# Kernel tuning notes

Measured on AMD Instinct MI355X. Metric: run time of the kernel, lower is better.

Reference implementation:

```python
import jax, jax.numpy as jnp
import numpy as np
from jax import lax

B, CI, CO, H, W = 8, 64, 64, 256, 256
M1 = M2 = 16
RANK, NEXP, SCALING = 4, 15, 0.1
G = 4  # expert_region_size = sqrt(num_experts + 1)
WF = W // 2 + 1

# expert i occupies grid cell (row, col) = ((i+1)//G, (i+1)%G); cell (0,0) is the base weights1 corner
_IDX = np.arange(1, NEXP + 1)
RR = jnp.asarray(_IDX // G)
CC = jnp.asarray(_IDX % G)


def setup_inputs() -> dict:
    key = jax.random.key(0)
    ks = jax.random.split(key, 20)
    rn = lambda k, shape, s: jax.random.normal(k, shape, jnp.float32) * s
    scale = 1.0 / (CI * CO)
    return {
        "x": rn(ks[0], (B, CI, H, W), 1.0),
        "w1_re": jax.random.uniform(ks[1], (CI, CO, M1, M2), jnp.float32) * scale,
        "w1_im": jax.random.uniform(ks[2], (CI, CO, M1, M2), jnp.float32) * scale,
        "w2_re": jax.random.uniform(ks[3], (CI, CO, M1, M2), jnp.float32) * scale,
        "w2_im": jax.random.uniform(ks[4], (CI, CO, M1, M2), jnp.float32) * scale,
        "la1_re": rn(ks[5], (NEXP, RANK, CI), 0.02),
        "la1_im": rn(ks[6], (NEXP, RANK, CI), 0.02),
        "lb1_re": rn(ks[7], (NEXP, CO, RANK, M1, M2), 0.02),
        "lb1_im": rn(ks[8], (NEXP, CO, RANK, M1, M2), 0.02),
        "la2_re": rn(ks[9], (NEXP, RANK, CI), 0.02),
        "la2_im": rn(ks[10], (NEXP, RANK, CI), 0.02),
        "lb2_re": rn(ks[11], (NEXP, CO, RANK, M1, M2), 0.02),
        "lb2_im": rn(ks[12], (NEXP, CO, RANK, M1, M2), 0.02),
        "gate1": rn(ks[13], (NEXP,), 0.1),
        "gate2": rn(ks[14], (NEXP,), 0.1),
    }


def reference(x, w1_re, w1_im, w2_re, w2_im,
              la1_re, la1_im, lb1_re, lb1_im,
              la2_re, la2_im, lb2_re, lb2_im,
              gate1, gate2):
    x_ft = jnp.fft.rfft2(x)  # [B, CI, H, WF] complex64

    # scalar gates (gate_on_data=False): sigmoid(gate / temperature), temperature=1
    g1 = jax.nn.sigmoid(gate1)  # [E]
    g2 = jax.nn.sigmoid(gate2)
    sploss = jnp.mean(g1) + jnp.mean(g2)

    w1 = lax.complex(w1_re, w1_im)
    w2 = lax.complex(w2_re, w2_im)
    la1 = lax.complex(la1_re, la1_im)
    lb1 = lax.complex(lb1_re, lb1_im)
    la2 = lax.complex(la2_re, la2_im)
    lb2 = lax.complex(lb2_re, lb2_im)

    # per-expert LoRA weights: sum_r lora_b[o,r,x,y] * lora_a[r,i] -> [E, I, O, M1, M2]
    lw1 = jnp.einsum("eri,eorxy->eioxy", la1, lb1) * SCALING
    lw2 = jnp.einsum("eri,eorxy->eioxy", la2, lb2) * SCALING

    # base corner products
    top_base = jnp.einsum("bixy,ioxy->boxy", x_ft[:, :, :M1, :M2], w1)
    bot_base = jnp.einsum("bixy,ioxy->boxy", x_ft[:, :, H - M1:, :M2], w2)

    # gather all expert input tiles at once via a GxG grid view of the low-freq corners
    top = x_ft[:, :, :G * M1, :G * M2].reshape(B, CI, G, M1, G, M2)
    topt = jnp.transpose(top, (2, 4, 0, 1, 3, 5))        # [G, G, B, CI, M1, M2]
    xe1 = topt[RR, CC]                                    # [E, B, CI, M1, M2]
    bot = x_ft[:, :, H - G * M1:, :G * M2].reshape(B, CI, G, M1, G, M2)
    bott = jnp.transpose(bot, (2, 4, 0, 1, 3, 5))
    xe2 = bott[G - 1 - RR, CC]  # rows H-row_end:H-row_start == bottom-grid block 3-row_idx

    oe1 = jnp.einsum("ebixy,eioxy->eboxy", xe1, lw1) * g1[:, None, None, None, None]
    oe2 = jnp.einsum("ebixy,eioxy->eboxy", xe2, lw2) * g2[:, None, None, None, None]

    # scatter all disjoint tiles back into out_ft
    out_top = jnp.zeros((G, G, B, CO, M1, M2), jnp.complex64)
    out_top = out_top.at[0, 0].set(top_base).at[RR, CC].set(oe1)
    out_bot = jnp.zeros((G, G, B, CO, M1, M2), jnp.complex64)
    out_bot = out_bot.at[G - 1, 0].set(bot_base).at[G - 1 - RR, CC].set(oe2)

    out_ft = jnp.zeros((B, CO, H, WF), jnp.complex64)
    top_full = jnp.transpose(out_top, (2, 3, 0, 4, 1, 5)).reshape(B, CO, G * M1, G * M2)
    bot_full = jnp.transpose(out_bot, (2, 3, 0, 4, 1, 5)).reshape(B, CO, G * M1, G * M2)
    out_ft = out_ft.at[:, :, :G * M1, :G * M2].set(top_full)
    out_ft = out_ft.at[:, :, H - G * M1:, :G * M2].set(bot_full)

    y = jnp.fft.irfft2(out_ft, s=(H, W))
    return (y, sploss)
```

## Files before the change

### kernel.cpp

```cpp
#include <hip/hip_runtime.h>
#include <math.h>

#define B_   8
#define CI_  64
#define CO_  64
#define H_   256
#define W_   256
#define NE_  15
#define RK_  4

typedef __attribute__((ext_vector_type(8))) short short8;
typedef __attribute__((ext_vector_type(4))) float f32x4;

__device__ __forceinline__ unsigned bf16u(float f) {
  return (__float_as_uint(f) + 0x8000u) >> 16;
}
__device__ __forceinline__ unsigned pk2(float lo, float hi) {
  return ((__float_as_uint(lo) + 0x8000u) >> 16) |
         ((__float_as_uint(hi) + 0x8000u) & 0xFFFF0000u);
}
__device__ __forceinline__ float ubf(unsigned short u) {
  return __uint_as_float(((unsigned)u) << 16);
}

__global__ __launch_bounds__(256) void kTab(unsigned short* __restrict__ TAt,
                                            unsigned short* __restrict__ TB,
                                            unsigned short* __restrict__ TD,
                                            unsigned short* __restrict__ TEt) {
  int idx = blockIdx.x * 256 + threadIdx.x;
  const float C = 6.28318530717958647692f / 256.f;
  if (idx < 32768) {
    int n = idx >> 8, q = idx & 255;
    int w = n >> 1, pl = n & 1;
    int mm = (q * w) & 255;
    float s, c; sincosf(C * (float)mm, &s, &c);
    TAt[idx] = (unsigned short)bf16u(pl ? -s : c);
    return;
  }
  idx -= 32768;
  if (idx < 131072) {
    int mrow = idx >> 9, k = idx & 511;
    int p = k >> 1, tt = k & 1;
    int hr = mrow & 127, imr = mrow >> 7;
    int h = (hr < 64) ? hr : hr + 128;
    int mm = (p * h) & 255;
    float s, c; sincosf(C * (float)mm, &s, &c);
    float v = (imr == 0) ? (tt == 0 ? c : s) : (tt == 0 ? -s : c);
    TB[idx] = (unsigned short)bf16u(v);
    return;
  }
  idx -= 131072;
  if (idx < 131072) {
    int mrow = idx >> 8, k = idx & 255;
    int hr = k >> 1, tt = k & 1;
    int p = mrow & 255, imr = mrow >> 8;
    int h = (hr < 64) ? hr : hr + 128;
    int mm = (p * h) & 255;
    float s, c; sincosf(C * (float)mm, &s, &c);
    float v = (imr == 0) ? (tt == 0 ? c : -s) : (tt == 0 ? s : c);
    TD[idx] = (unsigned short)bf16u(v);
    return;
  }
  idx -= 131072;
  if (idx < 32768) {
    int q = idx >> 7, k = idx & 127;
    int w = k >> 1, pl = k & 1;
    int mm = (q * w) & 255;
    float s, c; sincosf(C * (float)mm, &s, &c);
    float v = (pl == 0) ? ((w == 0 ? 1.f : 2.f * c) / 65536.f)
                        : ((w == 0 ? 0.f : -2.f * s) / 65536.f);
    TEt[idx] = (unsigned short)bf16u(v);
  }
}

__global__ __launch_bounds__(512, 4) void kAB(const float* __restrict__ x,
                                              const unsigned short* __restrict__ TAt,
                                              const unsigned short* __restrict__ TB,
                                              unsigned short* __restrict__ Xf) {
  __shared__ unsigned short As[256 * 32];
  __shared__ unsigned short Bs1[128 * 32];
  __shared__ unsigned short XcL[64 * 264];
  int t = threadIdx.x, lane = t & 63, wid = t >> 6;
  int bi = blockIdx.x;
  const float* xb = x + (size_t)bi * 65536;
  int lrow = lane & 15, lk = (lane >> 4) * 8;
  f32x4 acc2[2][4];
#pragma unroll
  for (int a = 0; a < 2; ++a)
#pragma unroll
    for (int b = 0; b < 4; ++b) acc2[a][b] = (f32x4){0.f, 0.f, 0.f, 0.f};

  for (int half = 0; half < 2; ++half) {
    f32x4 acc1[2][4];
#pragma unroll
    for (int a = 0; a < 2; ++a)
#pragma unroll
      for (int b = 0; b < 4; ++b) acc1[a][b] = (f32x4){0.f, 0.f, 0.f, 0.f};
    int mb1 = (wid >> 1) * 32, nb1 = (wid & 1) * 64;
    for (int kk = 0; kk < 8; ++kk) {
      int k0 = kk * 32;
      __syncthreads();
      {
        int r = t >> 2, hf = t & 3;
        const float* xp = xb + (size_t)(half * 128 + r) * 256 + k0 + hf * 8;
        float4 v0 = *(const float4*)(xp);
        float4 v1 = *(const float4*)(xp + 4);
        uint4 o;
        o.x = pk2(v0.x, v0.y); o.y = pk2(v0.z, v0.w);
        o.z = pk2(v1.x, v1.y); o.w = pk2(v1.z, v1.w);
        *(uint4*)&As[r * 32 + hf * 8] = o;
      }
      {
        int n = t >> 2, seg = t & 3;
        *(uint4*)&Bs1[n * 32 + seg * 8] = *(const uint4*)&TAt[n * 256 + k0 + seg * 8];
      }
      __syncthreads();
      short8 af[2], bf[4];
#pragma unroll
      for (int a = 0; a < 2; ++a)
        af[a] = *(const short8*)&As[(mb1 + a * 16 + lrow) * 32 + lk];
#pragma unroll
      for (int b = 0; b < 4; ++b)
        bf[b] = *(const short8*)&Bs1[(nb1 + b * 16 + lrow) * 32 + lk];
#pragma unroll
      for (int a = 0; a < 2; ++a)
#pragma unroll
        for (int b = 0; b < 4; ++b)
          acc1[a][b] = __builtin_amdgcn_mfma_f32_16x16x32_bf16(af[a], bf[b], acc1[a][b], 0, 0, 0);
    }
    __syncthreads();
#pragma unroll
    for (int a = 0; a < 2; ++a)
#pragma unroll
      for (int b = 0; b < 4; ++b)
#pragma unroll
        for (int r = 0; r < 4; ++r) {
          int m = mb1 + a * 16 + (lane >> 4) * 4 + r;
          int n = nb1 + b * 16 + lrow;
          XcL[(n >> 1) * 264 + 2 * m + (n & 1)] = (unsigned short)bf16u(acc1[a][b][r]);
        }
    __syncthreads();
    int mb2 = wid * 32;
    for (int kk = 0; kk < 8; ++kk) {
      int k0 = kk * 32;
      __syncthreads();
#pragma unroll
      for (int j = 0; j < 2; ++j) {
        int c = j * 512 + t;
        int m = c >> 2, seg = c & 3;
        *(uint4*)&As[m * 32 + seg * 8] =
            *(const uint4*)&TB[m * 512 + half * 256 + k0 + seg * 8];
      }
      __syncthreads();
      short8 af2[2], bf2[4];
#pragma unroll
      for (int a = 0; a < 2; ++a)
        af2[a] = *(const short8*)&As[(mb2 + a * 16 + lrow) * 32 + lk];
#pragma unroll
      for (int b = 0; b < 4; ++b)
        bf2[b] = *(const short8*)&XcL[(b * 16 + lrow) * 264 + k0 + lk];
#pragma unroll
      for (int a = 0; a < 2; ++a)
#pragma unroll
        for (int b = 0; b < 4; ++b)
          acc2[a][b] = __builtin_amdgcn_mfma_f32_16x16x32_bf16(af2[a], bf2[b], acc2[a][b], 0, 0, 0);
    }
  }
  unsigned short* dst = Xf + (size_t)bi * 16384;
#pragma unroll
  for (int a = 0; a < 2; ++a)
#pragma unroll
    for (int b = 0; b < 4; ++b)
#pragma unroll
      for (int r = 0; r < 4; ++r) {
        int m = wid * 32 + a * 16 + (lane >> 4) * 4 + r;
        int n = b * 16 + lrow;
        dst[m * 64 + n] = (unsigned short)bf16u(acc2[a][b][r]);
      }
}

__global__ __launch_bounds__(256) void kT(const unsigned short* __restrict__ Xf,
                                          float2* __restrict__ T,
                                          const float* __restrict__ la1re,
                                          const float* __restrict__ la1im,
                                          const float* __restrict__ la2re,
                                          const float* __restrict__ la2im) {
  int bid = blockIdx.x;
  int b = bid & 7;
  int e = (bid >> 3) % 15;
  int reg = bid / 120;
  int ep1 = e + 1;
  int grr = (reg == 0) ? (ep1 >> 2) : (3 - (ep1 >> 2));
  int gc = ep1 & 3;
  int hr0 = reg * 64 + grr * 16;
  int w0 = gc * 16;
  int t = threadIdx.x;
  int xx = t >> 4, yy = t & 15;
  const unsigned short* xp =
      Xf + (size_t)b * 64 * 16384 + (hr0 + xx) * 64 + (w0 + yy);
  const float* lare = (reg == 0) ? la1re : la2re;
  const float* laim = (reg == 0) ? la1im : la2im;
  float ar0 = 0.f, ai0 = 0.f, ar1 = 0.f, ai1 = 0.f;
  float ar2 = 0.f, ai2 = 0.f, ar3 = 0.f, ai3 = 0.f;
  for (int i = 0; i < 64; ++i) {
    float xr = ubf(xp[(size_t)i * 16384]);
    float xi = ubf(xp[(size_t)i * 16384 + 8192]);
    float l0r = lare[(e * 4 + 0) * 64 + i], l0i = laim[(e * 4 + 0) * 64 + i];
    float l1r = lare[(e * 4 + 1) * 64 + i], l1i = laim[(e * 4 + 1) * 64 + i];
    float l2r = lare[(e * 4 + 2) * 64 + i], l2i = laim[(e * 4 + 2) * 64 + i];
    float l3r = lare[(e * 4 + 3) * 64 + i], l3i = laim[(e * 4 + 3) * 64 + i];
    ar0 += l0r * xr - l0i * xi; ai0 += l0r * xi + l0i * xr;
    ar1 += l1r * xr - l1i * xi; ai1 += l1r * xi + l1i * xr;
    ar2 += l2r * xr - l2i * xi; ai2 += l2r * xi + l2i * xr;
    ar3 += l3r * xr - l3i * xi; ai3 += l3r * xi + l3i * xr;
  }
  float2* dst = T + ((((size_t)reg * 15 + e) * 8 + b) * 256 + t) * 4;
  dst[0] = make_float2(ar0, ai0);
  dst[1] = make_float2(ar1, ai1);
  dst[2] = make_float2(ar2, ai2);
  dst[3] = make_float2(ar3, ai3);
}

__global__ __launch_bounds__(256) void kD(const unsigned short* __restrict__ Xf,
                                          unsigned short* __restrict__ Gt,
                                          const float* __restrict__ w1re,
                                          const float* __restrict__ w1im,
                                          const float* __restrict__ w2re,
                                          const float* __restrict__ w2im) {
  __shared__ unsigned Xs[32 * 4 * 8 * 8];
  int bid = blockIdx.x;
  int yc = bid & 1, xc = (bid >> 1) & 3, oc = (bid >> 3) & 15, reg = bid >> 7;
  int hrb = (reg == 0) ? xc * 4 : 112 + xc * 4;
  const float* Wre = (reg == 0) ? w1re : w2re;
  const float* Wim = (reg == 0) ? w1im : w2im;
  int t = threadIdx.x;
  int b = t >> 5, o = (t >> 3) & 3, yy = t & 7;
  int og = oc * 4 + o, yyg = yc * 8 + yy;
  float ar[4] = {0.f, 0.f, 0.f, 0.f}, ai[4] = {0.f, 0.f, 0.f, 0.f};
  for (int ch = 0; ch < 2; ++ch) {
    __syncthreads();
#pragma unroll
    for (int j = 0; j < 4; ++j) {
      int seg = t + j * 256;
      int sb = seg >> 7, sx = (seg >> 5) & 3, si = seg & 31;
      int i = ch * 32 + si;
      const unsigned short* p =
          Xf + (size_t)(sb * 64 + i) * 16384 + (hrb + sx) * 64 + yc * 8;
      uint4 re = *(const uint4*)p;
      uint4 im = *(const uint4*)(p + 8192);
      uint4 o0, o1;
      o0.x = (re.x & 0xFFFFu) | (im.x << 16);
      o0.y = (re.x >> 16) | (im.x & 0xFFFF0000u);
      o0.z = (re.y & 0xFFFFu) | (im.y << 16);
      o0.w = (re.y >> 16) | (im.y & 0xFFFF0000u);
      o1.x = (re.z & 0xFFFFu) | (im.z << 16);
      o1.y = (re.z >> 16) | (im.z & 0xFFFF0000u);
      o1.z = (re.w & 0xFFFFu) | (im.w << 16);
      o1.w = (re.w >> 16) | (im.w & 0xFFFF0000u);
      uint4* d = (uint4*)&Xs[((si * 4 + sx) * 8 + sb) * 8];
      d[0] = o0; d[1] = o1;
    }
    __syncthreads();
    for (int ic = 0; ic < 32; ++ic) {
      int i = ch * 32 + ic;
#pragma unroll
      for (int xs = 0; xs < 4; ++xs) {
        unsigned pk = Xs[((ic * 4 + xs) * 8 + b) * 8 + yy];
        float xr = ubf((unsigned short)(pk & 0xFFFFu));
        float xi = ubf((unsigned short)(pk >> 16));
        int widx = ((i * 64 + og) * 16 + xc * 4 + xs) * 16 + yyg;
        float wr = Wre[widx], wi = Wim[widx];
        ar[xs] += xr * wr - xi * wi;
        ai[xs] += xr * wi + xi * wr;
      }
    }
  }
  uint4 ov;
  ov.x = pk2(ar[0], ai[0]);
  ov.y = pk2(ar[1], ai[1]);
  ov.z = pk2(ar[2], ai[2]);
  ov.w = pk2(ar[3], ai[3]);
  *(uint4*)(Gt + ((size_t)(b * 64 + og) * 64 + yyg) * 256 + 2 * hrb) = ov;
}

__global__ __launch_bounds__(256) void kM(const float2* __restrict__ T,
                                          unsigned short* __restrict__ Gt,
                                          const float* __restrict__ lb1re,
                                          const float* __restrict__ lb1im,
                                          const float* __restrict__ lb2re,
                                          const float* __restrict__ lb2im,
                                          const float* __restrict__ gate1,
                                          const float* __restrict__ gate2) {
  int bid = blockIdx.x;
  int xc = bid & 3, hrc = (bid >> 2) & 7, oc = bid >> 5;
  int t = threadIdx.x;
  int w = t & 63, og = t >> 6;
  int o = oc * 4 + og;
  int reg = hrc >> 2;
  int grr = hrc & 3;
  int gc = w >> 4, yy = w & 15;
  int e = (reg == 0) ? (4 * grr + gc - 1) : (4 * (3 - grr) + gc - 1);
  if (e < 0) return;
  float gate = (reg == 0) ? gate1[e] : gate2[e];
  float g = 0.1f / (1.f + __expf(-gate));
  const float* lbre = (reg == 0) ? lb1re : lb2re;
  const float* lbim = (reg == 0) ? lb1im : lb2im;
  size_t lbb = ((size_t)(e * 64 + o) * 4) * 256 + yy;
  float blr[4][4], bli[4][4];
#pragma unroll
  for (int x2 = 0; x2 < 4; ++x2) {
    int xx = xc * 4 + x2;
    const float* pr = lbre + lbb + xx * 16;
    const float* pi = lbim + lbb + xx * 16;
#pragma unroll
    for (int r = 0; r < 4; ++r) {
      blr[x2][r] = pr[r * 256];
      bli[x2][r] = pi[r * 256];
    }
  }
  const size_t tbase = (((size_t)reg * 15 + e) * 8) * 256 + yy;
  for (int b = 0; b < 8; ++b) {
    const float4* tp = (const float4*)(T + (tbase + (size_t)b * 256) * 4);
    unsigned out4[4];
#pragma unroll
    for (int x2 = 0; x2 < 4; ++x2) {
      int xx = xc * 4 + x2;
      float4 t01 = tp[xx * 32];
      float4 t23 = tp[xx * 32 + 1];
      float ar = 0.f, aim = 0.f;
      ar += t01.x * blr[x2][0] - t01.y * bli[x2][0];
      aim += t01.x * bli[x2][0] + t01.y * blr[x2][0];
      ar += t01.z * blr[x2][1] - t01.w * bli[x2][1];
      aim += t01.z * bli[x2][1] + t01.w * blr[x2][1];
      ar += t23.x * blr[x2][2] - t23.y * bli[x2][2];
      aim += t23.x * bli[x2][2] + t23.y * blr[x2][2];
      ar += t23.z * blr[x2][3] - t23.w * bli[x2][3];
      aim += t23.z * bli[x2][3] + t23.w * blr[x2][3];
      out4[x2] = pk2(g * ar, g * aim);
    }
    *(uint4*)(Gt + ((size_t)(b * 64 + o) * 64 + w) * 256 + hrc * 32 + xc * 8) =
        make_uint4(out4[0], out4[1], out4[2], out4[3]);
  }
}

__global__ __launch_bounds__(512) void kGD(const unsigned short* __restrict__ Gt,
                                           const unsigned short* __restrict__ TD,
                                           unsigned short* __restrict__ Zt) {
  __shared__ unsigned short As[512 * 32];
  __shared__ unsigned short Bs[64 * 32];
  int t = threadIdx.x, lane = t & 63, wid = t >> 6;
  int bo = blockIdx.x;
  const unsigned short* Grow = Gt + (size_t)bo * 16384;
  int mb = wid * 64;
  int lrow = lane & 15, lk = (lane >> 4) * 8;
  f32x4 acc[4][4];
#pragma unroll
  for (int a = 0; a < 4; ++a)
#pragma unroll
    for (int b = 0; b < 4; ++b) acc[a][b] = (f32x4){0.f, 0.f, 0.f, 0.f};

  for (int kk = 0; kk < 8; ++kk) {
    int k0 = kk * 32;
    __syncthreads();
#pragma unroll
    for (int j = 0; j < 4; ++j) {
      int c = j * 512 + t;
      int m = c >> 2, seg = c & 3;
      *(uint4*)&As[m * 32 + seg * 8] = *(const uint4*)&TD[m * 256 + k0 + seg * 8];
    }
    if (t < 256) {
      int n = t >> 2, seg = t & 3;
      *(uint4*)&Bs[n * 32 + seg * 8] = *(const uint4*)&Grow[n * 256 + k0 + seg * 8];
    }
    __syncthreads();
    short8 af[4], bf[4];
#pragma unroll
    for (int a = 0; a < 4; ++a)
      af[a] = *(const short8*)&As[(mb + a * 16 + lrow) * 32 + lk];
#pragma unroll
    for (int b = 0; b < 4; ++b)
      bf[b] = *(const short8*)&Bs[(b * 16 + lrow) * 32 + lk];
#pragma unroll
    for (int a = 0; a < 4; ++a)
#pragma unroll
      for (int b = 0; b < 4; ++b)
        acc[a][b] = __builtin_amdgcn_mfma_f32_16x16x32_bf16(af[a], bf[b], acc[a][b], 0, 0, 0);
  }
  unsigned short* dst = Zt + (size_t)bo * 32768;
#pragma unroll
  for (int a = 0; a < 4; ++a)
#pragma unroll
    for (int b = 0; b < 4; ++b)
#pragma unroll
      for (int r = 0; r < 4; ++r) {
        int m = mb + a * 16 + (lane >> 4) * 4 + r;
        int p = m & 255, pl = m >> 8;
        int n = b * 16 + lrow;
        dst[p * 128 + 2 * n + pl] = (unsigned short)bf16u(acc[a][b][r]);
      }
}

__global__ __launch_bounds__(512) void kGE(const unsigned short* __restrict__ Zt,
                                           const unsigned short* __restrict__ TEt,
                                           float* __restrict__ y) {
  __shared__ unsigned short As[256 * 32];
  __shared__ unsigned short Bs[128 * 32];
  int t = threadIdx.x, lane = t & 63, wid = t >> 6;
  int bo = blockIdx.x >> 1, qh = blockIdx.x & 1;
  const unsigned short* Zrow = Zt + (size_t)bo * 32768;
  int mb = (wid >> 1) * 64, nb = (wid & 1) * 64;
  int lrow = lane & 15, lk = (lane >> 4) * 8;
  f32x4 acc[4][4];
#pragma unroll
  for (int a = 0; a < 4; ++a)
#pragma unroll
    for (int b = 0; b < 4; ++b) acc[a][b] = (f32x4){0.f, 0.f, 0.f, 0.f};

  for (int kk = 0; kk < 4; ++kk) {
    int k0 = kk * 32;
    __syncthreads();
#pragma unroll
    for (int j = 0; j < 2; ++j) {
      int c = j * 512 + t;
      int m = c >> 2, seg = c & 3;
      *(uint4*)&As[m * 32 + seg * 8] = *(const uint4*)&Zrow[m * 128 + k0 + seg * 8];
    }
    {
      int n = t >> 2, seg = t & 3;
      *(uint4*)&Bs[n * 32 + seg * 8] =
          *(const uint4*)&TEt[(qh * 128 + n) * 128 + k0 + seg * 8];
    }
    __syncthreads();
    short8 af[4], bf[4];
#pragma unroll
    for (int a = 0; a < 4; ++a)
      af[a] = *(const short8*)&As[(mb + a * 16 + lrow) * 32 + lk];
#pragma unroll
    for (int b = 0; b < 4; ++b)
      bf[b] = *(const short8*)&Bs[(nb + b * 16 + lrow) * 32 + lk];
#pragma unroll
    for (int a = 0; a < 4; ++a)
#pragma unroll
      for (int b = 0; b < 4; ++b)
        acc[a][b] = __builtin_amdgcn_mfma_f32_16x16x32_bf16(af[a], bf[b], acc[a][b], 0, 0, 0);
  }
  float* dst = y + (size_t)bo * 65536 + qh * 128;
#pragma unroll
  for (int a = 0; a < 4; ++a)
#pragma unroll
    for (int b = 0; b < 4; ++b)
#pragma unroll
      for (int r = 0; r < 4; ++r) {
        int p = mb + a * 16 + (lane >> 4) * 4 + r;
        int q = nb + b * 16 + lrow;
        dst[(size_t)p * 256 + q] = acc[a][b][r];
      }
}

__global__ void kS2(const float* __restrict__ gate1, const float* __restrict__ gate2,
                    float* __restrict__ out) {
  if (threadIdx.x == 0) {
    float s = 0.f;
    for (int e = 0; e < NE_; ++e)
      s += 1.f / (1.f + expf(-gate1[e])) + 1.f / (1.f + expf(-gate2[e]));
    out[0] = s / (float)NE_;
  }
}

extern "C" void kernel_launch(void* const* d_in, const int* in_sizes, int n_in,
                              void* d_out, int out_size, void* d_ws, size_t ws_size,
                              hipStream_t stream) {
  const float* x     = (const float*)d_in[0];
  const float* w1re  = (const float*)d_in[1];
  const float* w1im  = (const float*)d_in[2];
  const float* w2re  = (const float*)d_in[3];
  const float* w2im  = (const float*)d_in[4];
  const float* la1re = (const float*)d_in[5];
  const float* la1im = (const float*)d_in[6];
  const float* lb1re = (const float*)d_in[7];
  const float* lb1im = (const float*)d_in[8];
  const float* la2re = (const float*)d_in[9];
  const float* la2im = (const float*)d_in[10];
  const float* lb2re = (const float*)d_in[11];
  const float* lb2im = (const float*)d_in[12];
  const float* gate1 = (const float*)d_in[13];
  const float* gate2 = (const float*)d_in[14];

  char* ws = (char*)d_ws;
  unsigned short* Xf  = (unsigned short*)(ws + ((size_t)32 << 20));
  unsigned short* Gt  = (unsigned short*)(ws + ((size_t)48 << 20));
  unsigned short* Zt  = (unsigned short*)(ws + ((size_t)64 << 20));
  unsigned short* TAt = (unsigned short*)(ws + ((size_t)96 << 20));
  unsigned short* TB  = TAt + 32768;
  unsigned short* TD  = TB + 131072;
  unsigned short* TEt = TD + 131072;
  float2* Tw = (float2*)(ws + ((size_t)97 << 20));
  float* y = (float*)d_out;

  kTab<<<1280, 256, 0, stream>>>(TAt, TB, TD, TEt);
  kAB<<<512, 512, 0, stream>>>(x, TAt, TB, Xf);
  kT<<<240, 256, 0, stream>>>(Xf, Tw, la1re, la1im, la2re, la2im);
  kD<<<256, 256, 0, stream>>>(Xf, Gt, w1re, w1im, w2re, w2im);
  kM<<<512, 256, 0, stream>>>(Tw, Gt, lb1re, lb1im, lb2re, lb2im, gate1, gate2);
  kGD<<<512, 512, 0, stream>>>(Gt, TD, Zt);
  kGE<<<1024, 512, 0, stream>>>(Zt, TEt, y);
  kS2<<<1, 64, 0, stream>>>(gate1, gate2, y + (size_t)B_ * CO_ * H_ * W_);
}
```

Before: 406.6 us.

## Fuse spectral mix kernels and chain inverse-FFT GEMMs through shared memory

Merges the base-weight mixing kernel and the LoRA expert kernel into one launch, with blocks branching by block index. It also fuses the two inverse-transform GEMMs so the intermediate Z tile stays in LDS (padded stride 136) and is no longer written to and read back from global memory. The fused GEMM kernel uses about 76 KB of shared memory per block, which may lower occupancy. Each block now does both GEMM stages serially, so the grid is 512 blocks instead of 512+1024.

```diff
diff --git a/kernel.cpp b/kernel.cpp
--- a/kernel.cpp
+++ b/kernel.cpp
@@ -221,240 +221,232 @@
   dst[3] = make_float2(ar3, ai3);
 }
 
-__global__ __launch_bounds__(256) void kD(const unsigned short* __restrict__ Xf,
-                                          unsigned short* __restrict__ Gt,
-                                          const float* __restrict__ w1re,
-                                          const float* __restrict__ w1im,
-                                          const float* __restrict__ w2re,
-                                          const float* __restrict__ w2im) {
+__global__ __launch_bounds__(256) void kDM(const unsigned short* __restrict__ Xf,
+                                           const float2* __restrict__ T,
+                                           unsigned short* __restrict__ Gt,
+                                           const float* __restrict__ w1re,
+                                           const float* __restrict__ w1im,
+                                           const float* __restrict__ w2re,
+                                           const float* __restrict__ w2im,
+                                           const float* __restrict__ lb1re,
+                                           const float* __restrict__ lb1im,
+                                           const float* __restrict__ lb2re,
+                                           const float* __restrict__ lb2im,
+                                           const float* __restrict__ gate1,
+                                           const float* __restrict__ gate2) {
   __shared__ unsigned Xs[32 * 4 * 8 * 8];
-  int bid = blockIdx.x;
-  int yc = bid & 1, xc = (bid >> 1) & 3, oc = (bid >> 3) & 15, reg = bid >> 7;
-  int hrb = (reg == 0) ? xc * 4 : 112 + xc * 4;
-  const float* Wre = (reg == 0) ? w1re : w2re;
-  const float* Wim = (reg == 0) ? w1im : w2im;
-  int t = threadIdx.x;
-  int b = t >> 5, o = (t >> 3) & 3, yy = t & 7;
-  int og = oc * 4 + o, yyg = yc * 8 + yy;
-  float ar[4] = {0.f, 0.f, 0.f, 0.f}, ai[4] = {0.f, 0.f, 0.f, 0.f};
-  for (int ch = 0; ch < 2; ++ch) {
-    __syncthreads();
-#pragma unroll
-    for (int j = 0; j < 4; ++j) {
-      int seg = t + j * 256;
-      int sb = seg >> 7, sx = (seg >> 5) & 3, si = seg & 31;
-      int i = ch * 32 + si;
-      const unsigned short* p =
-          Xf + (size_t)(sb * 64 + i) * 16384 + (hrb + sx) * 64 + yc * 8;
-      uint4 re = *(const uint4*)p;
-      uint4 im = *(const uint4*)(p + 8192);
-      uint4 o0, o1;
-      o0.x = (re.x & 0xFFFFu) | (im.x << 16);
-      o0.y = (re.x >> 16) | (im.x & 0xFFFF0000u);
-      o0.z = (re.y & 0xFFFFu) | (im.y << 16);
-      o0.w = (re.y >> 16) | (im.y & 0xFFFF0000u);
-      o1.x = (re.z & 0xFFFFu) | (im.z << 16);
-      o1.y = (re.z >> 16) | (im.z & 0xFFFF0000u);
-      o1.z = (re.w & 0xFFFFu) | (im.w << 16);
-      o1.w = (re.w >> 16) | (im.w & 0xFFFF0000u);
-      uint4* d = (uint4*)&Xs[((si * 4 + sx) * 8 + sb) * 8];
-      d[0] = o0; d[1] = o1;
-    }
-    __syncthreads();
-    for (int ic = 0; ic < 32; ++ic) {
-      int i = ch * 32 + ic;
-#pragma unroll
-      for (int xs = 0; xs < 4; ++xs) {
-        unsigned pk = Xs[((ic * 4 + xs) * 8 + b) * 8 + yy];
-        float xr = ubf((unsigned short)(pk & 0xFFFFu));
-        float xi = ubf((unsigned short)(pk >> 16));
-        int widx = ((i * 64 + og) * 16 + xc * 4 + xs) * 16 + yyg;
-        float wr = Wre[widx], wi = Wim[widx];
-        ar[xs] += xr * wr - xi * wi;
-        ai[xs] += xr * wi + xi * wr;
-      }
-    }
-  }
-  uint4 ov;
-  ov.x = pk2(ar[0], ai[0]);
-  ov.y = pk2(ar[1], ai[1]);
-  ov.z = pk2(ar[2], ai[2]);
-  ov.w = pk2(ar[3], ai[3]);
-  *(uint4*)(Gt + ((size_t)(b * 64 + og) * 64 + yyg) * 256 + 2 * hrb) = ov;
-}
-
-__global__ __launch_bounds__(256) void kM(const float2* __restrict__ T,
-                                          unsigned short* __restrict__ Gt,
-                                          const float* __restrict__ lb1re,
-                                          const float* __restrict__ lb1im,
-                                          const float* __restrict__ lb2re,
-                                          const float* __restrict__ lb2im,
-                                          const float* __restrict__ gate1,
-                                          const float* __restrict__ gate2) {
-  int bid = blockIdx.x;
-  int xc = bid & 3, hrc = (bid >> 2) & 7, oc = bid >> 5;
-  int t = threadIdx.x;
-  int w = t & 63, og = t >> 6;
-  int o = oc * 4 + og;
-  int reg = hrc >> 2;
-  int grr = hrc & 3;
-  int gc = w >> 4, yy = w & 15;
-  int e = (reg == 0) ? (4 * grr + gc - 1) : (4 * (3 - grr) + gc - 1);
-  if (e < 0) return;
-  float gate = (reg == 0) ? gate1[e] : gate2[e];
-  float g = 0.1f / (1.f + __expf(-gate));
-  const float* lbre = (reg == 0) ? lb1re : lb2re;
-  const float* lbim = (reg == 0) ? lb1im : lb2im;
-  size_t lbb = ((size_t)(e * 64 + o) * 4) * 256 + yy;
-  float blr[4][4], bli[4][4];
-#pragma unroll
-  for (int x2 = 0; x2 < 4; ++x2) {
-    int xx = xc * 4 + x2;
-    const float* pr = lbre + lbb + xx * 16;
-    const float* pi = lbim + lbb + xx * 16;
-#pragma unroll
-    for (int r = 0; r < 4; ++r) {
-      blr[x2][r] = pr[r * 256];
-      bli[x2][r] = pi[r * 256];
-    }
-  }
-  const size_t tbase = (((size_t)reg * 15 + e) * 8) * 256 + yy;
-  for (int b = 0; b < 8; ++b) {
-    const float4* tp = (const float4*)(T + (tbase + (size_t)b * 256) * 4);
-    unsigned out4[4];
+  if (blockIdx.x < 256) {
+    int bid = blockIdx.x;
+    int yc = bid & 1, xc = (bid >> 1) & 3, oc = (bid >> 3) & 15, reg = bid >> 7;
+    int hrb = (reg == 0) ? xc * 4 : 112 + xc * 4;
+    const float* Wre = (reg == 0) ? w1re : w2re;
+    const float* Wim = (reg == 0) ? w1im : w2im;
+    int t = threadIdx.x;
+    int b = t >> 5, o = (t >> 3) & 3, yy = t & 7;
+    int og = oc * 4 + o, yyg = yc * 8 + yy;
+    float ar[4] = {0.f, 0.f, 0.f, 0.f}, ai[4] = {0.f, 0.f, 0.f, 0.f};
+    for (int ch = 0; ch < 2; ++ch) {
+      __syncthreads();
+#pragma unroll
+      for (int j = 0; j < 4; ++j) {
+        int seg = t + j * 256;
+        int sb = seg >> 7, sx = (seg >> 5) & 3, si = seg & 31;
+        int i = ch * 32 + si;
+        const unsigned short* p =
+            Xf + (size_t)(sb * 64 + i) * 16384 + (hrb + sx) * 64 + yc * 8;
+        uint4 re = *(const uint4*)p;
+        uint4 im = *(const uint4*)(p + 8192);
+        uint4 o0, o1;
+        o0.x = (re.x & 0xFFFFu) | (im.x << 16);
+        o0.y = (re.x >> 16) | (im.x & 0xFFFF0000u);
+        o0.z = (re.y & 0xFFFFu) | (im.y << 16);
+        o0.w = (re.y >> 16) | (im.y & 0xFFFF0000u);
+        o1.x = (re.z & 0xFFFFu) | (im.z << 16);
+        o1.y = (re.z >> 16) | (im.z & 0xFFFF0000u);
+        o1.z = (re.w & 0xFFFFu) | (im.w << 16);
+        o1.w = (re.w >> 16) | (im.w & 0xFFFF0000u);
+        uint4* d = (uint4*)&Xs[((si * 4 + sx) * 8 + sb) * 8];
+        d[0] = o0; d[1] = o1;
+      }
+      __syncthreads();
+      for (int ic = 0; ic < 32; ++ic) {
+        int i = ch * 32 + ic;
+#pragma unroll
+        for (int xs = 0; xs < 4; ++xs) {
+          unsigned pk = Xs[((ic * 4 + xs) * 8 + b) * 8 + yy];
+          float xr = ubf((unsigned short)(pk & 0xFFFFu));
+          float xi = ubf((unsigned short)(pk >> 16));
+          int widx = ((i * 64 + og) * 16 + xc * 4 + xs) * 16 + yyg;
+          float wr = Wre[widx], wi = Wim[widx];
+          ar[xs] += xr * wr - xi * wi;
+          ai[xs] += xr * wi + xi * wr;
+        }
+      }
+    }
+    uint4 ov;
+    ov.x = pk2(ar[0], ai[0]);
+    ov.y = pk2(ar[1], ai[1]);
+    ov.z = pk2(ar[2], ai[2]);
+    ov.w = pk2(ar[3], ai[3]);
+    *(uint4*)(Gt + ((size_t)(b * 64 + og) * 64 + yyg) * 256 + 2 * hrb) = ov;
+  } else {
+    int bid = blockIdx.x - 256;
+    int xc = bid & 3, hrc = (bid >> 2) & 7, oc = bid >> 5;
+    int t = threadIdx.x;
+    int w = t & 63, og = t >> 6;
+    int o = oc * 4 + og;
+    int reg = hrc >> 2;
+    int grr = hrc & 3;
+    int gc = w >> 4, yy = w & 15;
+    int e = (reg == 0) ? (4 * grr + gc - 1) : (4 * (3 - grr) + gc - 1);
+    if (e < 0) return;
+    float gate = (reg == 0) ? gate1[e] : gate2[e];
+    float g = 0.1f / (1.f + __expf(-gate));
+    const float* lbre = (reg == 0) ? lb1re : lb2re;
+    const float* lbim = (reg == 0) ? lb1im : lb2im;
+    size_t lbb = ((size_t)(e * 64 + o) * 4) * 256 + yy;
+    float blr[4][4], bli[4][4];
 #pragma unroll
     for (int x2 = 0; x2 < 4; ++x2) {
       int xx = xc * 4 + x2;
-      float4 t01 = tp[xx * 32];
-      float4 t23 = tp[xx * 32 + 1];
-      float ar = 0.f, aim = 0.f;
-      ar += t01.x * blr[x2][0] - t01.y * bli[x2][0];
-      aim += t01.x * bli[x2][0] + t01.y * blr[x2][0];
-      ar += t01.z * blr[x2][1] - t01.w * bli[x2][1];
-      aim += t01.z * bli[x2][1] + t01.w * blr[x2][1];
-      ar += t23.x * blr[x2][2] - t23.y * bli[x2][2];
-      aim += t23.x * bli[x2][2] + t23.y * blr[x2][2];
-      ar += t23.z * blr[x2][3] - t23.w * bli[x2][3];
-      aim += t23.z * bli[x2][3] + t23.w * blr[x2][3];
-      out4[x2] = pk2(g * ar, g * aim);
-    }
-    *(uint4*)(Gt + ((size_t)(b * 64 + o) * 64 + w) * 256 + hrc * 32 + xc * 8) =
-        make_uint4(out4[0], out4[1], out4[2], out4[3]);
-  }
-}
-
-__global__ __launch_bounds__(512) void kGD(const unsigned short* __restrict__ Gt,
-                                           const unsigned short* __restrict__ TD,
-                                           unsigned short* __restrict__ Zt) {
-  __shared__ unsigned short As[512 * 32];
-  __shared__ unsigned short Bs[64 * 32];
+      const float* pr = lbre + lbb + xx * 16;
+      const float* pi = lbim + lbb + xx * 16;
+#pragma unroll
+      for (int r = 0; r < 4; ++r) {
+        blr[x2][r] = pr[r * 256];
+        bli[x2][r] = pi[r * 256];
+      }
+    }
+    const size_t tbase = (((size_t)reg * 15 + e) * 8) * 256 + yy;
+    for (int b = 0; b < 8; ++b) {
+      const float4* tp = (const float4*)(T + (tbase + (size_t)b * 256) * 4);
+      unsigned out4[4];
+#pragma unroll
+      for (int x2 = 0; x2 < 4; ++x2) {
+        int xx = xc * 4 + x2;
+        float4 t01 = tp[xx * 32];
+        float4 t23 = tp[xx * 32 + 1];
+        float ar = 0.f, aim = 0.f;
+        ar += t01.x * blr[x2][0] - t01.y * bli[x2][0];
+        aim += t01.x * bli[x2][0] + t01.y * blr[x2][0];
+        ar += t01.z * blr[x2][1] - t01.w * bli[x2][1];
+        aim += t01.z * bli[x2][1] + t01.w * blr[x2][1];
+        ar += t23.x * blr[x2][2] - t23.y * bli[x2][2];
+        aim += t23.x * bli[x2][2] + t23.y * blr[x2][2];
+        ar += t23.z * blr[x2][3] - t23.w * bli[x2][3];
+        aim += t23.z * bli[x2][3] + t23.w * blr[x2][3];
+        out4[x2] = pk2(g * ar, g * aim);
+      }
+      *(uint4*)(Gt + ((size_t)(b * 64 + o) * 64 + w) * 256 + hrc * 32 + xc * 8) =
+          make_uint4(out4[0], out4[1], out4[2], out4[3]);
+    }
+  }
+}
+
+__global__ __launch_bounds__(512, 4) void kDE(const unsigned short* __restrict__ Gt,
+                                              const unsigned short* __restrict__ TD,
+                                              const unsigned short* __restrict__ TEt,
+                                              float* __restrict__ y) {
+  __shared__ __align__(16) char smem[77824];
+  unsigned short* As  = (unsigned short*)smem;
+  unsigned short* Bs  = (unsigned short*)(smem + 32768);
+  unsigned short* ZL  = (unsigned short*)smem;
+  unsigned short* Bs2 = (unsigned short*)(smem + 69632);
   int t = threadIdx.x, lane = t & 63, wid = t >> 6;
   int bo = blockIdx.x;
   const unsigned short* Grow = Gt + (size_t)bo * 16384;
-  int mb = wid * 64;
   int lrow = lane & 15, lk = (lane >> 4) * 8;
-  f32x4 acc[4][4];
-#pragma unroll
-  for (int a = 0; a < 4; ++a)
-#pragma unroll
-    for (int b = 0; b < 4; ++b) acc[a][b] = (f32x4){0.f, 0.f, 0.f, 0.f};
-
-  for (int kk = 0; kk < 8; ++kk) {
-    int k0 = kk * 32;
+
+  {
+    int mb = wid * 64;
+    f32x4 acc[4][4];
+#pragma unroll
+    for (int a = 0; a < 4; ++a)
+#pragma unroll
+      for (int b = 0; b < 4; ++b) acc[a][b] = (f32x4){0.f, 0.f, 0.f, 0.f};
+    for (int kk = 0; kk < 8; ++kk) {
+      int k0 = kk * 32;
+      __syncthreads();
+#pragma unroll
+      for (int j = 0; j < 4; ++j) {
+        int c = j * 512 + t;
+        int m = c >> 2, seg = c & 3;
+        *(uint4*)&As[m * 32 + seg * 8] = *(const uint4*)&TD[m * 256 + k0 + seg * 8];
+      }
+      if (t < 256) {
+        int n = t >> 2, seg = t & 3;
+        *(uint4*)&Bs[n * 32 + seg * 8] = *(const uint4*)&Grow[n * 256 + k0 + seg * 8];
+      }
+      __syncthreads();
+      short8 af[4], bf[4];
+#pragma unroll
+      for (int a = 0; a < 4; ++a)
+        af[a] = *(const short8*)&As[(mb + a * 16 + lrow) * 32 + lk];
+#pragma unroll
+      for (int b = 0; b < 4; ++b)
+        bf[b] = *(const short8*)&Bs[(b * 16 + lrow) * 32 + lk];
+#pragma unroll
+      for (int a = 0; a < 4; ++a)
+#pragma unroll
+        for (int b = 0; b < 4; ++b)
+          acc[a][b] = __builtin_amdgcn_mfma_f32_16x16x32_bf16(af[a], bf[b], acc[a][b], 0, 0, 0);
+    }
     __syncthreads();
 #pragma unroll
-    for (int j = 0; j < 4; ++j) {
-      int c = j * 512 + t;
-      int m = c >> 2, seg = c & 3;
-      *(uint4*)&As[m * 32 + seg * 8] = *(const uint4*)&TD[m * 256 + k0 + seg * 8];
-    }
-    if (t < 256) {
-      int n = t >> 2, seg = t & 3;
-      *(uint4*)&Bs[n * 32 + seg * 8] = *(const uint4*)&Grow[n * 256 + k0 + seg * 8];
-    }
+    for (int a = 0; a < 4; ++a)
+#pragma unroll
+      for (int b = 0; b < 4; ++b)
+#pragma unroll
+        for (int r = 0; r < 4; ++r) {
+          int m = mb + a * 16 + (lane >> 4) * 4 + r;
+          int p = m & 255, pl = m >> 8;
+          int n = b * 16 + lrow;
+          ZL[p * 136 + 2 * n + pl] = (unsigned short)bf16u(acc[a][b][r]);
+        }
     __syncthreads();
-    short8 af[4], bf[4];
+  }
+
+  int mb2 = (wid >> 1) * 64, nb2 = (wid & 1) * 64;
+  for (int qh = 0; qh < 2; ++qh) {
+    f32x4 acc[4][4];
 #pragma unroll
     for (int a = 0; a < 4; ++a)
-      af[a] = *(const short8*)&As[(mb + a * 16 + lrow) * 32 + lk];
-#pragma unroll
-    for (int b = 0; b < 4; ++b)
-      bf[b] = *(const short8*)&Bs[(b * 16 + lrow) * 32 + lk];
+#pragma unroll
+      for (int b = 0; b < 4; ++b) acc[a][b] = (f32x4){0.f, 0.f, 0.f, 0.f};
+    for (int kk = 0; kk < 4; ++kk) {
+      int k0 = kk * 32;
+      __syncthreads();
+      {
+        int n = t >> 2, seg = t & 3;
+        *(uint4*)&Bs2[n * 32 + seg * 8] =
+            *(const uint4*)&TEt[(qh * 128 + n) * 128 + k0 + seg * 8];
+      }
+      __syncthreads();
+      short8 af[4], bf[4];
+#pragma unroll
+      for (int a = 0; a < 4; ++a)
+        af[a] = *(const short8*)&ZL[(mb2 + a * 16 + lrow) * 136 + k0 + lk];
+#pragma unroll
+      for (int b = 0; b < 4; ++b)
+        bf[b] = *(const short8*)&Bs2[(nb2 + b * 16 + lrow) * 32 + lk];
+#pragma unroll
+      for (int a = 0; a < 4; ++a)
+#pragma unroll
+        for (int b = 0; b < 4; ++b)
+          acc[a][b] = __builtin_amdgcn_mfma_f32_16x16x32_bf16(af[a], bf[b], acc[a][b], 0, 0, 0);
+    }
+    float* dst = y + (size_t)bo * 65536 + qh * 128;
 #pragma unroll
     for (int a = 0; a < 4; ++a)
 #pragma unroll
       for (int b = 0; b < 4; ++b)
-        acc[a][b] = __builtin_amdgcn_mfma_f32_16x16x32_bf16(af[a], bf[b], acc[a][b], 0, 0, 0);
-  }
-  unsigned short* dst = Zt + (size_t)bo * 32768;
-#pragma unroll
-  for (int a = 0; a < 4; ++a)
-#pragma unroll
-    for (int b = 0; b < 4; ++b)
-#pragma unroll
-      for (int r = 0; r < 4; ++r) {
-        int m = mb + a * 16 + (lane >> 4) * 4 + r;
-        int p = m & 255, pl = m >> 8;
-        int n = b * 16 + lrow;
-        dst[p * 128 + 2 * n + pl] = (unsigned short)bf16u(acc[a][b][r]);
-      }
-}
-
-__global__ __launch_bounds__(512) void kGE(const unsigned short* __restrict__ Zt,
-                                           const unsigned short* __restrict__ TEt,
-                                           float* __restrict__ y) {
-  __shared__ unsigned short As[256 * 32];
-  __shared__ unsigned short Bs[128 * 32];
-  int t = threadIdx.x, lane = t & 63, wid = t >> 6;
-  int bo = blockIdx.x >> 1, qh = blockIdx.x & 1;
-  const unsigned short* Zrow = Zt + (size_t)bo * 32768;
-  int mb = (wid >> 1) * 64, nb = (wid & 1) * 64;
-  int lrow = lane & 15, lk = (lane >> 4) * 8;
-  f32x4 acc[4][4];
-#pragma unroll
-  for (int a = 0; a < 4; ++a)
-#pragma unroll
-    for (int b = 0; b < 4; ++b) acc[a][b] = (f32x4){0.f, 0.f, 0.f, 0.f};
-
-  for (int kk = 0; kk < 4; ++kk) {
-    int k0 = kk * 32;
-    __syncthreads();
-#pragma unroll
-    for (int j = 0; j < 2; ++j) {
-      int c = j * 512 + t;
-      int m = c >> 2, seg = c & 3;
-      *(uint4*)&As[m * 32 + seg * 8] = *(const uint4*)&Zrow[m * 128 + k0 + seg * 8];
-    }
-    {
-      int n = t >> 2, seg = t & 3;
-      *(uint4*)&Bs[n * 32 + seg * 8] =
-          *(const uint4*)&TEt[(qh * 128 + n) * 128 + k0 + seg * 8];
-    }
-    __syncthreads();
-    short8 af[4], bf[4];
-#pragma unroll
-    for (int a = 0; a < 4; ++a)
-      af[a] = *(const short8*)&As[(mb + a * 16 + lrow) * 32 + lk];
-#pragma unroll
-    for (int b = 0; b < 4; ++b)
-      bf[b] = *(const short8*)&Bs[(nb + b * 16 + lrow) * 32 + lk];
-#pragma unroll
-    for (int a = 0; a < 4; ++a)
-#pragma unroll
-      for (int b = 0; b < 4; ++b)
-        acc[a][b] = __builtin_amdgcn_mfma_f32_16x16x32_bf16(af[a], bf[b], acc[a][b], 0, 0, 0);
-  }
-  float* dst = y + (size_t)bo * 65536 + qh * 128;
-#pragma unroll
-  for (int a = 0; a < 4; ++a)
-#pragma unroll
-    for (int b = 0; b < 4; ++b)
-#pragma unroll
-      for (int r = 0; r < 4; ++r) {
-        int p = mb + a * 16 + (lane >> 4) * 4 + r;
-        int q = nb + b * 16 + lrow;
-        dst[(size_t)p * 256 + q] = acc[a][b][r];
-      }
+#pragma unroll
+        for (int r = 0; r < 4; ++r) {
+          int p = mb2 + a * 16 + (lane >> 4) * 4 + r;
+          int q = nb2 + b * 16 + lrow;
+          dst[(size_t)p * 256 + q] = acc[a][b][r];
+        }
+  }
 }
 
 __global__ void kS2(const float* __restrict__ gate1, const float* __restrict__ gate2,
@@ -489,7 +481,6 @@
   char* ws = (char*)d_ws;
   unsigned short* Xf  = (unsigned short*)(ws + ((size_t)32 << 20));
   unsigned short* Gt  = (unsigned short*)(ws + ((size_t)48 << 20));
-  unsigned short* Zt  = (unsigned short*)(ws + ((size_t)64 << 20));
   unsigned short* TAt = (unsigned short*)(ws + ((size_t)96 << 20));
   unsigned short* TB  = TAt + 32768;
   unsigned short* TD  = TB + 131072;
@@ -500,9 +491,8 @@
   kTab<<<1280, 256, 0, stream>>>(TAt, TB, TD, TEt);
   kAB<<<512, 512, 0, stream>>>(x, TAt, TB, Xf);
   kT<<<240, 256, 0, stream>>>(Xf, Tw, la1re, la1im, la2re, la2im);
-  kD<<<256, 256, 0, stream>>>(Xf, Gt, w1re, w1im, w2re, w2im);
-  kM<<<512, 256, 0, stream>>>(Tw, Gt, lb1re, lb1im, lb2re, lb2im, gate1, gate2);
-  kGD<<<512, 512, 0, stream>>>(Gt, TD, Zt);
-  kGE<<<1024, 512, 0, stream>>>(Zt, TEt, y);
+  kDM<<<768, 256, 0, stream>>>(Xf, Tw, Gt, w1re, w1im, w2re, w2im,
+                               lb1re, lb1im, lb2re, lb2im, gate1, gate2);
+  kDE<<<512, 512, 0, stream>>>(Gt, TD, TEt, y);
   kS2<<<1, 64, 0, stream>>>(gate1, gate2, y + (size_t)B_ * CO_ * H_ * W_);
 }
```

Result: faster. 395.9 us (-2.7%).
